# Performance work log

Hardware: AMD Instinct MI355X
Metric: run time of the kernel (lower is better)

## Reference

```python
import jax, jax.numpy as jnp
import numpy as np

D_IN = 1024
D_OUT = 1024


def setup_inputs() -> dict:
    key = jax.random.key(0)
    kx, kq, kk, kv = jax.random.split(key, 4)
    s = 1.0 / np.sqrt(D_IN)
    x = jax.random.normal(kx, (2, 4096, D_IN), dtype=jnp.float32)
    # nn.Linear weights: shape [d_out, d_in], y = x @ W.T (no bias)
    W_query = jax.random.normal(kq, (D_OUT, D_IN), dtype=jnp.float32) * s
    W_key = jax.random.normal(kk, (D_OUT, D_IN), dtype=jnp.float32) * s
    W_value = jax.random.normal(kv, (D_OUT, D_IN), dtype=jnp.float32) * s
    return {"x": x, "W_query": W_query, "W_key": W_key, "W_value": W_value}


def reference(x, W_query, W_key, W_value):
    # QKV projections: [b, n, d_in] @ [d_in, d_out]
    q = jnp.einsum('bnd,od->bno', x, W_query)
    k = jnp.einsum('bnd,od->bno', x, W_key)
    v = jnp.einsum('bnd,od->bno', x, W_value)
    d_k = k.shape[-1]
    scores = jnp.einsum('bqo,bko->bqk', q, k) / jnp.sqrt(jnp.asarray(d_k, x.dtype))
    # NOTE: source applies no causal mask despite the class name
    attn = jax.nn.softmax(scores, axis=-1)
    return jnp.einsum('bqk,bko->bqo', attn, v)
```

## Files before the change

kernel.cpp:

```cpp
#include <hip/hip_runtime.h>
#include <hip/hip_bf16.h>
#include <hip/hip_fp16.h>
#include <stdint.h>

typedef __bf16 bf16_t;
typedef __bf16 bf16x8 __attribute__((ext_vector_type(8)));
typedef float f32x4 __attribute__((ext_vector_type(4)));

typedef __attribute__((address_space(1))) void gv_t;
typedef __attribute__((address_space(3))) void lv_t;

__device__ inline unsigned short f2bf_bits(float f) {
  uint32_t u = __float_as_uint(f);
  u += 0x7FFFu + ((u >> 16) & 1u);
  return (unsigned short)(u >> 16);
}
__device__ inline bf16_t f2bf(float f) {
  unsigned short h = f2bf_bits(f);
  return __builtin_bit_cast(bf16_t, h);
}

__device__ inline void storeC(float* p, float v) { *p = v; }
__device__ inline void storeC(bf16_t* p, float v) { *p = f2bf(v); }
__device__ inline void storeC(__half* p, float v) { *p = __float2half(v); }

__global__ __launch_bounds__(256)
void convert_all(const float* __restrict__ x, const float* __restrict__ wq,
                 const float* __restrict__ wk, const float* __restrict__ wv,
                 bf16_t* __restrict__ xb, bf16_t* __restrict__ wqkb,
                 bf16_t* __restrict__ wvb)
{
  const int64_t NX = 8192LL * 1024, NW = 1024LL * 1024;
  const int64_t total4 = (NX + 3 * NW) >> 2;
  for (int64_t i = (int64_t)blockIdx.x * blockDim.x + threadIdx.x; i < total4;
       i += (int64_t)gridDim.x * blockDim.x) {
    int64_t e = i << 2;
    const float* src; bf16_t* dst; int64_t off;
    if (e < NX)               { src = x;  dst = xb;         off = e; }
    else if (e < NX + NW)     { src = wq; dst = wqkb;       off = e - NX; }
    else if (e < NX + 2 * NW) { src = wk; dst = wqkb + NW;  off = e - NX - NW; }
    else                      { src = wv; dst = wvb;        off = e - NX - 2 * NW; }
    float4 f = *(const float4*)(src + off);
    uint32_t lo = ((uint32_t)f2bf_bits(f.y) << 16) | f2bf_bits(f.x);
    uint32_t hi = ((uint32_t)f2bf_bits(f.w) << 16) | f2bf_bits(f.z);
    *(uint2*)(dst + off) = make_uint2(lo, hi);
  }
}

template <typename OUT_T>
__global__ __launch_bounds__(256)
void gemm_bt(const bf16_t* __restrict__ A, const bf16_t* __restrict__ B,
             OUT_T* __restrict__ C, int K, int lda, int ldb, int ldc,
             int64_t b_batch_stride, int bm_per_batch)
{
  __shared__ bf16_t As[2][128 * 32];
  __shared__ bf16_t Bs[2][128 * 32];
  const int tid  = threadIdx.x;
  const int wid  = tid >> 6;
  const int lane = tid & 63;
  const int wm = wid >> 1, wn = wid & 1;
  const int64_t bm = blockIdx.x;
  const int64_t bn = blockIdx.y;

  const bf16_t* Bb = B + (bm / bm_per_batch) * b_batch_stride;

  const int c0row = (wid * 2 + 0) * 16 + (lane >> 2);
  const int c1row = (wid * 2 + 1) * 16 + (lane >> 2);
  const int scol  = (lane & 3) * 8;

  const bf16_t* Ar0 = A  + (bm * 128 + c0row) * lda + scol;
  const bf16_t* Ar1 = A  + (bm * 128 + c1row) * lda + scol;
  const bf16_t* Br0 = Bb + (bn * 128 + c0row) * ldb + scol;
  const bf16_t* Br1 = Bb + (bn * 128 + c1row) * ldb + scol;

  const int ad0 = (wid * 2 + 0) * 512;
  const int ad1 = (wid * 2 + 1) * 512;

  const int frow = lane & 15;
  const int fk   = (lane >> 4) * 8;
  const int aoff = (wm * 64 + frow) * 32 + fk;
  const int boff = (wn * 64 + frow) * 32 + fk;

  f32x4 acc[4][4];
  #pragma unroll
  for (int m = 0; m < 4; m++)
    #pragma unroll
    for (int n = 0; n < 4; n++) acc[m][n] = f32x4{0.f, 0.f, 0.f, 0.f};

  auto stage = [&](int buf, int k0) {
    __builtin_amdgcn_global_load_lds((const gv_t*)(Ar0 + k0),
                                     (lv_t*)(&As[buf][ad0]), 16, 0, 0);
    __builtin_amdgcn_global_load_lds((const gv_t*)(Ar1 + k0),
                                     (lv_t*)(&As[buf][ad1]), 16, 0, 0);
    __builtin_amdgcn_global_load_lds((const gv_t*)(Br0 + k0),
                                     (lv_t*)(&Bs[buf][ad0]), 16, 0, 0);
    __builtin_amdgcn_global_load_lds((const gv_t*)(Br1 + k0),
                                     (lv_t*)(&Bs[buf][ad1]), 16, 0, 0);
  };

  stage(0, 0);
  __syncthreads();
  int cur = 0;
  for (int k0 = 0; k0 < K; k0 += 32) {
    if (k0 + 32 < K) stage(cur ^ 1, k0 + 32);

    bf16x8 af[4], bfr[4];
    #pragma unroll
    for (int m = 0; m < 4; m++)
      af[m] = *(const bf16x8*)(&As[cur][aoff + m * 16 * 32]);
    #pragma unroll
    for (int n = 0; n < 4; n++)
      bfr[n] = *(const bf16x8*)(&Bs[cur][boff + n * 16 * 32]);
    #pragma unroll
    for (int m = 0; m < 4; m++)
      #pragma unroll
      for (int n = 0; n < 4; n++)
        acc[m][n] = __builtin_amdgcn_mfma_f32_16x16x32_bf16(af[m], bfr[n],
                                                            acc[m][n], 0, 0, 0);
    __syncthreads();
    cur ^= 1;
  }

  const int crow = (lane >> 4) * 4;
  const int ccol = lane & 15;
  #pragma unroll
  for (int m = 0; m < 4; m++)
    #pragma unroll
    for (int n = 0; n < 4; n++)
      #pragma unroll
      for (int j = 0; j < 4; j++) {
        int64_t row = bm * 128 + wm * 64 + m * 16 + crow + j;
        int64_t col = bn * 128 + wn * 64 + n * 16 + ccol;
        storeC(&C[row * ldc + col], acc[m][n][j]);
      }
}

template <typename OUT_T, typename OUT2_T>
__global__ __launch_bounds__(512, 2)
void gemm256(const bf16_t* __restrict__ A, const bf16_t* __restrict__ B,
             OUT_T* __restrict__ C0, OUT2_T* __restrict__ C1,
             int K, int lda, int ldb, int ldc,
             int64_t b_batch_stride, int bm_per_batch,
             int64_t za_off, int64_t zb_off)
{
  __shared__ bf16_t As[2][256][64];
  __shared__ bf16_t Bs[2][256][64];

  const int tid  = threadIdx.x;
  const int wid  = tid >> 6;
  const int lane = tid & 63;
  const int wm = wid >> 2;
  const int wn = wid & 3;
  const int64_t bm = blockIdx.x;
  const int64_t bn = blockIdx.y;
  const int z = blockIdx.z;

  const bf16_t* Ap = A + (int64_t)z * za_off;
  const bf16_t* Bp = B + (bm / bm_per_batch) * b_batch_stride
                       + (int64_t)z * zb_off;

  const int srow  = wid * 16 + (lane >> 3);
  const int sslot = (lane & 7) ^ (lane >> 3);
  const int64_t lda64 = lda, ldb64 = ldb;
  const bf16_t* Ag = Ap + (bm * 256 + srow) * lda64 + sslot * 8;
  const bf16_t* Bg = Bp + (bn * 256 + srow) * ldb64 + sslot * 8;

  auto stageA = [&](int buf, int t, int h) {
    const bf16_t* src = Ag + (int64_t)(h * 128) * lda64 + t * 64;
    char* dst = (char*)&As[buf][h * 128 + wid * 16][0];
    __builtin_amdgcn_global_load_lds((const gv_t*)src, (lv_t*)dst, 16, 0, 0);
    __builtin_amdgcn_global_load_lds((const gv_t*)(src + 8 * lda64),
                                     (lv_t*)(dst + 1024), 16, 0, 0);
  };
  auto stageB = [&](int buf, int t, int h) {
    const bf16_t* src = Bg + (int64_t)(h * 128) * ldb64 + t * 64;
    char* dst = (char*)&Bs[buf][h * 128 + wid * 16][0];
    __builtin_amdgcn_global_load_lds((const gv_t*)src, (lv_t*)dst, 16, 0, 0);
    __builtin_amdgcn_global_load_lds((const gv_t*)(src + 8 * ldb64),
                                     (lv_t*)(dst + 1024), 16, 0, 0);
  };

  const int frow   = lane & 15;
  const int fcol16 = lane >> 4;
  const int xorv   = (lane & 7) << 4;
  const int ck0 = (fcol16 * 16) ^ xorv;
  const int ck1 = (64 + fcol16 * 16) ^ xorv;
  const int arowb = (wm * 128 + frow) * 128;
  const int browb = (wn * 64  + frow) * 128;

  f32x4 acc[8][4];
  #pragma unroll
  for (int m = 0; m < 8; m++)
    #pragma unroll
    for (int n = 0; n < 4; n++) acc[m][n] = f32x4{0.f, 0.f, 0.f, 0.f};

  const int NT = K >> 6;

  stageA(0, 0, 0); stageA(0, 0, 1);
  stageB(0, 0, 0); stageB(0, 0, 1);
  stageB(1, 1, 0); stageB(1, 1, 1);
  asm volatile("s_waitcnt vmcnt(4)" ::: "memory");
  __builtin_amdgcn_s_barrier();
  __builtin_amdgcn_sched_barrier(0);

  bf16x8 a[8][2], bb[4][2];

  for (int g = 0; g < NT; ++g) {
    const int buf = g & 1;
    const char* lA = (const char*)&As[buf][0][0];
    const char* lB = (const char*)&Bs[buf][0][0];

    #pragma unroll
    for (int m = 0; m < 8; m++) {
      a[m][0] = *(const bf16x8*)(lA + arowb + m * 2048 + ck0);
      a[m][1] = *(const bf16x8*)(lA + arowb + m * 2048 + ck1);
    }
    #pragma unroll
    for (int n = 0; n < 4; n++) {
      bb[n][0] = *(const bf16x8*)(lB + browb + n * 2048 + ck0);
      bb[n][1] = *(const bf16x8*)(lB + browb + n * 2048 + ck1);
    }
    if (g + 1 < NT) stageA(buf ^ 1, g + 1, 0);
    __builtin_amdgcn_s_barrier();
    __builtin_amdgcn_s_setprio(1);
    #pragma unroll
    for (int m = 0; m < 4; m++)
      #pragma unroll
      for (int n = 0; n < 2; n++)
        #pragma unroll
        for (int k = 0; k < 2; k++)
          acc[m][n] = __builtin_amdgcn_mfma_f32_16x16x32_bf16(a[m][k], bb[n][k],
                                                              acc[m][n], 0, 0, 0);
    __builtin_amdgcn_s_setprio(0);
    __builtin_amdgcn_s_barrier();

    if (g + 1 < NT) stageA(buf ^ 1, g + 1, 1);
    __builtin_amdgcn_s_barrier();
    __builtin_amdgcn_s_setprio(1);
    #pragma unroll
    for (int m = 0; m < 4; m++)
      #pragma unroll
      for (int n = 2; n < 4; n++)
        #pragma unroll
        for (int k = 0; k < 2; k++)
          acc[m][n] = __builtin_amdgcn_mfma_f32_16x16x32_bf16(a[m][k], bb[n][k],
                                                              acc[m][n], 0, 0, 0);
    __builtin_amdgcn_s_setprio(0);
    __builtin_amdgcn_s_barrier();

    if (g + 2 < NT) stageB(buf, g + 2, 0);
    __builtin_amdgcn_s_barrier();
    __builtin_amdgcn_s_setprio(1);
    #pragma unroll
    for (int m = 4; m < 8; m++)
      #pragma unroll
      for (int n = 0; n < 2; n++)
        #pragma unroll
        for (int k = 0; k < 2; k++)
          acc[m][n] = __builtin_amdgcn_mfma_f32_16x16x32_bf16(
              a[m][k], bb[n][k], acc[m][n], 0, 0, 0);
    __builtin_amdgcn_s_setprio(0);
    __builtin_amdgcn_s_barrier();

    if (g + 2 < NT) stageB(buf, g + 2, 1);
    __builtin_amdgcn_s_barrier();
    __builtin_amdgcn_s_setprio(1);
    #pragma unroll
    for (int m = 4; m < 8; m++)
      #pragma unroll
      for (int n = 2; n < 4; n++)
        #pragma unroll
        for (int k = 0; k < 2; k++)
          acc[m][n] = __builtin_amdgcn_mfma_f32_16x16x32_bf16(
              a[m][k], bb[n][k], acc[m][n], 0, 0, 0);
    __builtin_amdgcn_s_setprio(0);
    if (g + 2 < NT) {
      asm volatile("s_waitcnt vmcnt(4)" ::: "memory");
    } else {
      asm volatile("s_waitcnt vmcnt(0)" ::: "memory");
    }
    __builtin_amdgcn_s_barrier();
    __builtin_amdgcn_sched_barrier(0);
  }

  const int crow = (lane >> 4) * 4;
  const int ccol = lane & 15;
  if (z == 0) {
    #pragma unroll
    for (int m = 0; m < 8; m++)
      #pragma unroll
      for (int n = 0; n < 4; n++)
        #pragma unroll
        for (int j = 0; j < 4; j++) {
          int64_t row = bm * 256 + wm * 128 + m * 16 + crow + j;
          int64_t col = bn * 256 + wn * 64 + n * 16 + ccol;
          storeC(&C0[row * (int64_t)ldc + col], acc[m][n][j]);
        }
  } else {
    #pragma unroll
    for (int m = 0; m < 8; m++)
      #pragma unroll
      for (int n = 0; n < 4; n++)
        #pragma unroll
        for (int j = 0; j < 4; j++) {
          int64_t row = bm * 256 + wm * 128 + m * 16 + crow + j;
          int64_t col = bn * 256 + wn * 64 + n * 16 + ccol;
          storeC(&C1[row * (int64_t)ldc + col], acc[m][n][j]);
        }
  }
}

__global__ __launch_bounds__(256)
void softmax_rows(__half* __restrict__ SP)
{
  const int64_t row = blockIdx.x;
  __half* s = SP + row * 4096;
  bf16_t* p = (bf16_t*)s;
  const int tid = threadIdx.x;
  const float scale = 0.03125f;

  float v[16];
  float vmax = -3.4e38f;
  #pragma unroll
  for (int i = 0; i < 4; i++) {
    uint2 raw = *(const uint2*)(s + i * 1024 + tid * 4);
    __half2 h01 = __builtin_bit_cast(__half2, raw.x);
    __half2 h23 = __builtin_bit_cast(__half2, raw.y);
    float2 f01 = __half22float2(h01);
    float2 f23 = __half22float2(h23);
    v[i * 4 + 0] = f01.x * scale;
    v[i * 4 + 1] = f01.y * scale;
    v[i * 4 + 2] = f23.x * scale;
    v[i * 4 + 3] = f23.y * scale;
    vmax = fmaxf(vmax, fmaxf(fmaxf(v[i*4+0], v[i*4+1]),
                             fmaxf(v[i*4+2], v[i*4+3])));
  }
  #pragma unroll
  for (int o = 32; o > 0; o >>= 1) vmax = fmaxf(vmax, __shfl_xor(vmax, o));
  __shared__ float redm[4];
  __shared__ float reds[4];
  if ((tid & 63) == 0) redm[tid >> 6] = vmax;
  __syncthreads();
  vmax = fmaxf(fmaxf(redm[0], redm[1]), fmaxf(redm[2], redm[3]));

  float lsum = 0.f;
  #pragma unroll
  for (int i = 0; i < 16; i++) {
    v[i] = __expf(v[i] - vmax);
    lsum += v[i];
  }
  #pragma unroll
  for (int o = 32; o > 0; o >>= 1) lsum += __shfl_xor(lsum, o);
  if ((tid & 63) == 0) reds[tid >> 6] = lsum;
  __syncthreads();
  lsum = (reds[0] + reds[1]) + (reds[2] + reds[3]);
  const float inv = 1.0f / lsum;

  #pragma unroll
  for (int i = 0; i < 4; i++) {
    uint32_t lo = ((uint32_t)f2bf_bits(v[i*4+1] * inv) << 16) | f2bf_bits(v[i*4+0] * inv);
    uint32_t hi = ((uint32_t)f2bf_bits(v[i*4+3] * inv) << 16) | f2bf_bits(v[i*4+2] * inv);
    *(uint2*)(p + i * 1024 + tid * 4) = make_uint2(lo, hi);
  }
}

__global__ __launch_bounds__(256)
void addk_h4(float4* __restrict__ o, const uint2* __restrict__ a, int64_t n4)
{
  for (int64_t i = (int64_t)blockIdx.x * blockDim.x + threadIdx.x; i < n4;
       i += (int64_t)gridDim.x * blockDim.x) {
    float4 x = o[i];
    uint2 raw = a[i];
    __half2 h01 = __builtin_bit_cast(__half2, raw.x);
    __half2 h23 = __builtin_bit_cast(__half2, raw.y);
    float2 f01 = __half22float2(h01);
    float2 f23 = __half22float2(h23);
    x.x += f01.x; x.y += f01.y; x.z += f23.x; x.w += f23.y;
    o[i] = x;
  }
}

extern "C" void kernel_launch(void* const* d_in, const int* in_sizes, int n_in,
                              void* d_out, int out_size, void* d_ws, size_t ws_size,
                              hipStream_t stream) {
  const float* x  = (const float*)d_in[0];
  const float* wq = (const float*)d_in[1];
  const float* wk = (const float*)d_in[2];
  const float* wv = (const float*)d_in[3];
  float* out = (float*)d_out;

  char* ws = (char*)d_ws;
  bf16_t* xb   = (bf16_t*)ws;
  bf16_t* wqkb = (bf16_t*)(ws + (16LL << 20));
  bf16_t* wvb  = (bf16_t*)(ws + (20LL << 20));
  __half* S    = (__half*)ws;
  bf16_t* qk   = (bf16_t*)(ws + (64LL << 20));
  __half* pk16 = (__half*)(ws + (64LL << 20));
  bf16_t* vt   = (bf16_t*)(ws + (96LL << 20));

  const int NO_BATCH = 1 << 30;

  convert_all<<<2048, 256, 0, stream>>>(x, wq, wk, wv, xb, wqkb, wvb);

  gemm256<bf16_t, bf16_t><<<dim3(32, 8, 1), 512, 0, stream>>>(
      xb, wqkb, qk, qk, 1024, 1024, 1024, 2048, 0, NO_BATCH, 0, 0);

  gemm_bt<bf16_t><<<dim3(8, 64), 256, 0, stream>>>(
      wvb, xb, vt, 1024, 1024, 1024, 8192, 0, NO_BATCH);

  gemm256<__half, __half><<<dim3(32, 16, 1), 512, 0, stream>>>(
      qk, qk + 1024, S, S, 1024, 2048, 2048, 4096, 4096LL * 2048, 16, 0, 0);

  softmax_rows<<<8192, 256, 0, stream>>>(S);

  gemm256<float, __half><<<dim3(32, 4, 2), 512, 0, stream>>>(
      (const bf16_t*)S, vt, out, pk16, 2048, 4096, 8192, 1024,
      4096, 16, 2048, 2048);

  addk_h4<<<2048, 256, 0, stream>>>((float4*)out, (const uint2*)pk16,
                                    8192LL * 1024 / 4);
}
```

Measured before the change: 247.3 us.

## Simplify GEMM main loop to single-stage double buffering with one barrier

Replaces the four-phase interleaved schedule with a plain double buffer. That schedule staged A one tile ahead and B two tiles ahead, with barriers between MFMA quarters. Each iteration now reads all LDS fragments, issues every global-to-LDS load for the next tile, runs all 64 MFMAs in one block, then waits for vmcnt(0) and hits a single barrier. This cuts barrier count and scheduling complexity. The cost is a shallower prefetch distance for B and a full memory-wait stall each iteration, so load latency may be less hidden.

```diff
diff --git a/kernel.cpp b/kernel.cpp
--- a/kernel.cpp
+++ b/kernel.cpp
@@ -198,8 +198,7 @@
 
   stageA(0, 0, 0); stageA(0, 0, 1);
   stageB(0, 0, 0); stageB(0, 0, 1);
-  stageB(1, 1, 0); stageB(1, 1, 1);
-  asm volatile("s_waitcnt vmcnt(4)" ::: "memory");
+  asm volatile("s_waitcnt vmcnt(0)" ::: "memory");
   __builtin_amdgcn_s_barrier();
   __builtin_amdgcn_sched_barrier(0);
 
@@ -211,74 +210,35 @@
     const char* lB = (const char*)&Bs[buf][0][0];
 
     #pragma unroll
-    for (int m = 0; m < 8; m++) {
+    for (int m = 0; m < 8; m++)
       a[m][0] = *(const bf16x8*)(lA + arowb + m * 2048 + ck0);
+    #pragma unroll
+    for (int n = 0; n < 4; n++)
+      bb[n][0] = *(const bf16x8*)(lB + browb + n * 2048 + ck0);
+    #pragma unroll
+    for (int m = 0; m < 8; m++)
       a[m][1] = *(const bf16x8*)(lA + arowb + m * 2048 + ck1);
+    #pragma unroll
+    for (int n = 0; n < 4; n++)
+      bb[n][1] = *(const bf16x8*)(lB + browb + n * 2048 + ck1);
+
+    if (g + 1 < NT) {
+      stageA(buf ^ 1, g + 1, 0); stageA(buf ^ 1, g + 1, 1);
+      stageB(buf ^ 1, g + 1, 0); stageB(buf ^ 1, g + 1, 1);
     }
-    #pragma unroll
-    for (int n = 0; n < 4; n++) {
-      bb[n][0] = *(const bf16x8*)(lB + browb + n * 2048 + ck0);
-      bb[n][1] = *(const bf16x8*)(lB + browb + n * 2048 + ck1);
-    }
-    if (g + 1 < NT) stageA(buf ^ 1, g + 1, 0);
-    __builtin_amdgcn_s_barrier();
+
     __builtin_amdgcn_s_setprio(1);
     #pragma unroll
-    for (int m = 0; m < 4; m++)
-      #pragma unroll
-      for (int n = 0; n < 2; n++)
+    for (int k = 0; k < 2; k++)
+      #pragma unroll
+      for (int m = 0; m < 8; m++)
         #pragma unroll
-        for (int k = 0; k < 2; k++)
-          acc[m][n] = __builtin_amdgcn_mfma_f32_16x16x32_bf16(a[m][k], bb[n][k],
-                                                              acc[m][n], 0, 0, 0);
-    __builtin_amdgcn_s_setprio(0);
-    __builtin_amdgcn_s_barrier();
-
-    if (g + 1 < NT) stageA(buf ^ 1, g + 1, 1);
-    __builtin_amdgcn_s_barrier();
-    __builtin_amdgcn_s_setprio(1);
-    #pragma unroll
-    for (int m = 0; m < 4; m++)
-      #pragma unroll
-      for (int n = 2; n < 4; n++)
-        #pragma unroll
-        for (int k = 0; k < 2; k++)
-          acc[m][n] = __builtin_amdgcn_mfma_f32_16x16x32_bf16(a[m][k], bb[n][k],
-                                                              acc[m][n], 0, 0, 0);
-    __builtin_amdgcn_s_setprio(0);
-    __builtin_amdgcn_s_barrier();
-
-    if (g + 2 < NT) stageB(buf, g + 2, 0);
-    __builtin_amdgcn_s_barrier();
-    __builtin_amdgcn_s_setprio(1);
-    #pragma unroll
-    for (int m = 4; m < 8; m++)
-      #pragma unroll
-      for (int n = 0; n < 2; n++)
-        #pragma unroll
-        for (int k = 0; k < 2; k++)
+        for (int n = 0; n < 4; n++)
           acc[m][n] = __builtin_amdgcn_mfma_f32_16x16x32_bf16(
               a[m][k], bb[n][k], acc[m][n], 0, 0, 0);
     __builtin_amdgcn_s_setprio(0);
-    __builtin_amdgcn_s_barrier();
-
-    if (g + 2 < NT) stageB(buf, g + 2, 1);
-    __builtin_amdgcn_s_barrier();
-    __builtin_amdgcn_s_setprio(1);
-    #pragma unroll
-    for (int m = 4; m < 8; m++)
-      #pragma unroll
-      for (int n = 2; n < 4; n++)
-        #pragma unroll
-        for (int k = 0; k < 2; k++)
-          acc[m][n] = __builtin_amdgcn_mfma_f32_16x16x32_bf16(
-              a[m][k], bb[n][k], acc[m][n], 0, 0, 0);
-    __builtin_amdgcn_s_setprio(0);
-    if (g + 2 < NT) {
-      asm volatile("s_waitcnt vmcnt(4)" ::: "memory");
-    } else {
-      asm volatile("s_waitcnt vmcnt(0)" ::: "memory");
-    }
+
+    asm volatile("s_waitcnt vmcnt(0)" ::: "memory");
     __builtin_amdgcn_s_barrier();
     __builtin_amdgcn_sched_barrier(0);
   }
```

After: 230.6 us. 6.8% less time.
